# Kernel optimization log

Measured on AMD Instinct MI355X. Metric: run time of the kernel, lower is better.

Reference implementation:

```python
import jax, jax.numpy as jnp
import numpy as np

NUM_HEADS = 8
EPS = 1e-5


def conv3x3(x, w):
    # x: (b,c,f,w), w: (out_c,in_c,3,3), padding=1, stride=1, no bias
    return jax.lax.conv_general_dilated(
        x, w, window_strides=(1, 1), padding=((1, 1), (1, 1)),
        dimension_numbers=('NCHW', 'OIHW', 'NCHW'))


def mc_layernorm(x, g, b):
    # MultichannelLayerNorm: layernorm over the feature axis (dim 2),
    # per-(channel, feature) affine.
    m = jnp.mean(x, axis=2, keepdims=True)
    v = jnp.var(x, axis=2, keepdims=True)
    xn = (x - m) * jax.lax.rsqrt(v + EPS)
    return xn * g[None, :, :, None] + b[None, :, :, None]


def mc_linear(x, wp, wd=None):
    # per-channel feature linear: y[b,c,g,w] = sum_f wp[c,g,f] x[b,c,f,w]
    y = jnp.einsum('bcfw,cgf->bcgw', x, wp)
    if wd is not None:  # depthwise=True adds 1x1 cross-channel mix
        y = jnp.einsum('bcfw,oc->bofw', y, wd)
    return y


def _split_heads(t):
    # (b,c,f,w) -> (b,c,w,H,dh); matches transpose(2,3).reshape(b,c,w,H,-1)
    b, c, f, w = t.shape
    return jnp.transpose(t, (0, 1, 3, 2)).reshape(b, c, w, NUM_HEADS, f // NUM_HEADS)


def _forward(x, conv_q, conv_k, conv_v, wq, wk, wv, wo_pw, wo_dw,
             g1, b1, g2, b2, w1_pw, w1_dw, w2_pw):
    b, c, f, w = x.shape
    # --- attention (MultichannelMultiheadAttention, prev_qk=None) ---
    n1 = mc_layernorm(x, g1, b1)
    q = _split_heads(mc_linear(conv3x3(n1, conv_q), wq))  # (b,c,w,H,dh)
    k = _split_heads(mc_linear(conv3x3(n1, conv_k), wk))
    v = _split_heads(mc_linear(conv3x3(n1, conv_v), wv))
    # qk: (b,c,H,w,w); scaled by sqrt(features) (torch uses sqrt(h)=height)
    qk = jnp.einsum('bcqhd,bckhd->bchqk', q, k) / jnp.sqrt(jnp.float32(f))
    a = jnp.einsum('bchqk,bckhd->bcqhd', jax.nn.softmax(qk, axis=-1), v)
    a = jnp.transpose(a.reshape(b, c, w, f), (0, 1, 3, 2))  # (b,c,f,w)
    z = mc_linear(a, wo_pw, wo_dw)  # o_proj, depthwise=True
    h = x + z  # dropout is identity in eval
    # --- FFN with SquaredReLU ---
    n2 = mc_layernorm(h, g2, b2)
    u = mc_linear(n2, w1_pw, w1_dw)          # (b,c,4f,w)
    u = jnp.square(jax.nn.relu(u))           # SquaredReLU
    z = mc_linear(u, w2_pw)                  # (b,c,f,w)
    h = h + z
    return h, qk


def setup_inputs() -> dict:
    key = jax.random.key(0)
    ks = jax.random.split(key, 12)
    b, c, f, w = 2, 16, 256, 512
    e = 4 * f
    s_conv = 1.0 / np.sqrt(c * 9)
    s_f = 1.0 / np.sqrt(f)
    s_e = 1.0 / np.sqrt(e)
    s_c = 1.0 / np.sqrt(c)
    return {
        'x': jax.random.normal(ks[0], (b, c, f, w), jnp.float32),
        'conv_q': jax.random.normal(ks[1], (c, c, 3, 3), jnp.float32) * s_conv,
        'conv_k': jax.random.normal(ks[2], (c, c, 3, 3), jnp.float32) * s_conv,
        'conv_v': jax.random.normal(ks[3], (c, c, 3, 3), jnp.float32) * s_conv,
        'wq': jax.random.normal(ks[4], (c, f, f), jnp.float32) * s_f,
        'wk': jax.random.normal(ks[5], (c, f, f), jnp.float32) * s_f,
        'wv': jax.random.normal(ks[6], (c, f, f), jnp.float32) * s_f,
        'wo_pw': jax.random.normal(ks[7], (c, f, f), jnp.float32) * s_f,
        'wo_dw': jax.random.normal(ks[8], (c, c), jnp.float32) * s_c,
        'g1': jnp.ones((c, f), jnp.float32),
        'b1': jnp.zeros((c, f), jnp.float32),
        'g2': jnp.ones((c, f), jnp.float32),
        'b2': jnp.zeros((c, f), jnp.float32),
        'w1_pw': jax.random.normal(ks[9], (c, e, f), jnp.float32) * s_f,
        'w1_dw': jax.random.normal(ks[10], (c, c), jnp.float32) * s_c,
        'w2_pw': jax.random.normal(ks[11], (c, f, e), jnp.float32) * s_e,
    }


def reference(x, conv_q, conv_k, conv_v, wq, wk, wv, wo_pw, wo_dw,
              g1, b1, g2, b2, w1_pw, w1_dw, w2_pw):
    return _forward(x, conv_q, conv_k, conv_v, wq, wk, wv, wo_pw, wo_dw,
                    g1, b1, g2, b2, w1_pw, w1_dw, w2_pw)
```

## Files before the change

### kernel.cpp

```cpp
#include <hip/hip_runtime.h>

#define BB 2
#define CC 16
#define BC 32
#define FF 256
#define WW 512
#define HH 8
#define DH 32

using bf16x8 = __attribute__((ext_vector_type(8))) __bf16;
using f32x4  = __attribute__((ext_vector_type(4))) float;
using us8    = __attribute__((ext_vector_type(8))) unsigned short;
using us4    = __attribute__((ext_vector_type(4))) unsigned short;

#define AS1 __attribute__((address_space(1)))
#define AS3 __attribute__((address_space(3)))

__device__ __forceinline__ float bf2f(unsigned short u) {
    union { unsigned int i; float f; } x; x.i = ((unsigned int)u) << 16; return x.f;
}
__device__ __forceinline__ unsigned short f2bf(float f) {
    union { float f; unsigned int i; } x; x.f = f;
    unsigned int r = x.i + 0x7fffu + ((x.i >> 16) & 1u);
    return (unsigned short)(r >> 16);
}
__device__ __forceinline__ f32x4 mfma16(bf16x8 a, bf16x8 b, f32x4 c) {
    return __builtin_amdgcn_mfma_f32_16x16x32_bf16(a, b, c, 0, 0, 0);
}
__device__ __forceinline__ void gload16(const void* g, void* l) {
    __builtin_amdgcn_global_load_lds((AS1 void*)g, (AS3 void*)l, 16, 0, 0);
}

__global__ __launch_bounds__(256) void prep_ln(
    const float* __restrict__ x, const float* __restrict__ g1,
    const float* __restrict__ b1, unsigned short* __restrict__ n1,
    const float* __restrict__ wq, const float* __restrict__ wk,
    const float* __restrict__ wv, const float* __restrict__ wo,
    const float* __restrict__ w1, const float* __restrict__ w2,
    const float* __restrict__ cwq, const float* __restrict__ cwk,
    const float* __restrict__ cwv,
    unsigned short* __restrict__ Wqkv, unsigned short* __restrict__ Wo16,
    unsigned short* __restrict__ W116, unsigned short* __restrict__ W216,
    unsigned short* __restrict__ Aw) {
    __shared__ float red[2][8][32];
    __shared__ float mr[2][32];
    int bid = blockIdx.x;
    if (bid < 512) {
        int bc = bid & 31, c = bc & 15;
        int part = threadIdx.x >> 5, wl = threadIdx.x & 31;
        int w = (bid >> 5) * 32 + wl;
        const float* xp = x + ((size_t)bc * FF + part * 32) * WW + w;
        float s = 0.f, s2 = 0.f;
#pragma unroll 4
        for (int i = 0; i < 32; ++i) { float t = xp[(size_t)i * WW]; s += t; s2 += t * t; }
        red[0][part][wl] = s; red[1][part][wl] = s2;
        __syncthreads();
        if (part == 0) {
            float S = 0.f, S2 = 0.f;
#pragma unroll
            for (int p = 0; p < 8; ++p) { S += red[0][p][wl]; S2 += red[1][p][wl]; }
            float m = S * (1.f / FF);
            float v = S2 * (1.f / FF) - m * m;
            mr[0][wl] = m; mr[1][wl] = rsqrtf(v + 1e-5f);
        }
        __syncthreads();
        float m = mr[0][wl], r = mr[1][wl];
        const float* gp = g1 + c * FF + part * 32;
        const float* bp = b1 + c * FF + part * 32;
        unsigned short* op = n1 + ((size_t)bc * FF + part * 32) * WW + w;
#pragma unroll 4
        for (int i = 0; i < 32; ++i)
            op[(size_t)i * WW] = f2bf((xp[(size_t)i * WW] - m) * r * gp[i] + bp[i]);
    } else if (bid < 512 + 6144) {
        int i = (bid - 512) * 256 + threadIdx.x;
        const float* s; unsigned short* d; int off;
        if (i < 131072)       { s = wq; d = Wqkv;            off = i; }
        else if (i < 262144)  { s = wk; d = Wqkv + 1048576;  off = i - 131072; }
        else if (i < 393216)  { s = wv; d = Wqkv + 2097152;  off = i - 262144; }
        else if (i < 524288)  { s = wo; d = Wo16;            off = i - 393216; }
        else if (i < 1048576) { s = w1; d = W116;            off = i - 524288; }
        else                  { s = w2; d = W216;            off = i - 1048576; }
        const float4* sp = (const float4*)s + (size_t)off * 2;
        float4 a = sp[0], b = sp[1];
        us8 p;
        p[0] = f2bf(a.x); p[1] = f2bf(a.y); p[2] = f2bf(a.z); p[3] = f2bf(a.w);
        p[4] = f2bf(b.x); p[5] = f2bf(b.y); p[6] = f2bf(b.z); p[7] = f2bf(b.w);
        *((us8*)d + off) = p;
    } else {
        int idx = (bid - 512 - 6144) * 256 + threadIdx.x;
        if (idx < 7680) {
            int tensor = idx / 2560;
            int r = idx - tensor * 2560;
            int tp = r >> 9, co = (r >> 5) & 15, k = r & 31;
            int tap = tp * 2 + (k >> 4), ci = k & 15;
            float v = 0.f;
            if (tap < 9) {
                const float* w = tensor == 0 ? cwq : (tensor == 1 ? cwk : cwv);
                v = w[(co * 16 + ci) * 9 + tap];
            }
            Aw[idx] = f2bf(v);
        }
    }
}

__global__ __launch_bounds__(256) void ln2t_kernel(
    const float* __restrict__ x, const float* __restrict__ g,
    const float* __restrict__ bta, unsigned short* __restrict__ out) {
    __shared__ float red[2][8][32];
    __shared__ float mr[2][32];
    int bc = blockIdx.x, c = bc & 15;
    int part = threadIdx.x >> 5, wl = threadIdx.x & 31;
    int w = blockIdx.y * 32 + wl;
    const float* xp = x + ((size_t)bc * FF + part * 32) * WW + w;
    float s = 0.f, s2 = 0.f;
#pragma unroll 4
    for (int i = 0; i < 32; ++i) { float t = xp[(size_t)i * WW]; s += t; s2 += t * t; }
    red[0][part][wl] = s; red[1][part][wl] = s2;
    __syncthreads();
    if (part == 0) {
        float S = 0.f, S2 = 0.f;
#pragma unroll
        for (int p = 0; p < 8; ++p) { S += red[0][p][wl]; S2 += red[1][p][wl]; }
        float m = S * (1.f / FF);
        float v = S2 * (1.f / FF) - m * m;
        mr[0][wl] = m; mr[1][wl] = rsqrtf(v + 1e-5f);
    }
    __syncthreads();
    float m = mr[0][wl], r = mr[1][wl];
    const float* gp = g + c * FF + part * 32;
    const float* bp = bta + c * FF + part * 32;
    unsigned short* op = out + ((size_t)bc * WW + w) * FF + part * 32;
    for (int i8 = 0; i8 < 4; ++i8) {
        us8 pk;
#pragma unroll
        for (int e = 0; e < 8; ++e) {
            int i = i8 * 8 + e;
            pk[e] = f2bf((xp[(size_t)i * WW] - m) * r * gp[i] + bp[i]);
        }
        *(us8*)(op + i8 * 8) = pk;
    }
}

__global__ __launch_bounds__(256) void conv3_mfma(
    const unsigned short* __restrict__ n1, const unsigned short* __restrict__ Aw,
    unsigned short* __restrict__ oq, unsigned short* __restrict__ ok,
    unsigned short* __restrict__ ov) {
    __shared__ __align__(16) unsigned short Xl[6][68][16];
    const int b = blockIdx.z;
    const int f0 = blockIdx.y * 4;
    const int w0 = blockIdx.x * 64;
    const int tx = threadIdx.x;
    const int lane = tx & 63, wid = tx >> 6;
    const int lr = lane & 15, lg = lane >> 4;
    {
        uint4 z{0, 0, 0, 0};
        for (int i = tx; i < 816; i += 256) ((uint4*)Xl)[i] = z;
    }
    __syncthreads();
    if (tx < 240) {
        int c = tx % 10;
        int fr = (tx / 10) % 6;
        int ci0 = (tx / 60) * 4;
        int fy = f0 - 1 + fr;
        int wx = w0 - 8 + c * 8;
        if (fy >= 0 && fy < FF && wx >= 0 && wx <= WW - 8) {
            const unsigned short* base = n1 + ((size_t)(b * CC + ci0) * FF + fy) * WW + wx;
            us8 v0 = *(const us8*)(base);
            us8 v1 = *(const us8*)(base + (size_t)FF * WW);
            us8 v2 = *(const us8*)(base + (size_t)2 * FF * WW);
            us8 v3 = *(const us8*)(base + (size_t)3 * FF * WW);
            if (c >= 1 && c <= 8) {
#pragma unroll
                for (int e = 0; e < 8; ++e) {
                    int wl = c * 8 + e - 7;
                    us4 p; p.x = v0[e]; p.y = v1[e]; p.z = v2[e]; p.w = v3[e];
                    *(us4*)(&Xl[fr][wl][ci0]) = p;
                }
            } else {
#pragma unroll
                for (int e = 0; e < 8; ++e) {
                    int wl = c * 8 + e - 7;
                    if (wl >= 0 && wl < 66) {
                        us4 p; p.x = v0[e]; p.y = v1[e]; p.z = v2[e]; p.w = v3[e];
                        *(us4*)(&Xl[fr][wl][ci0]) = p;
                    }
                }
            }
        }
    }
    __syncthreads();
    bf16x8 A[3][5];
#pragma unroll
    for (int t3 = 0; t3 < 3; ++t3)
#pragma unroll
        for (int t = 0; t < 5; ++t)
            A[t3][t] = *(const bf16x8*)(Aw + ((t3 * 5 + t) * 16 + lr) * 32 + lg * 8);
    const bool h = (lane & 32) != 0;
    int doff[5];
    doff[0] = (h ? (-68 * 32) : ((-68 - 1) * 32));
    doff[1] = (h ? (-1 * 32) : ((-68 + 1) * 32));
    doff[2] = (h ? (1 * 32) : 0);
    doff[3] = (h ? (68 * 32) : ((68 - 1) * 32));
    doff[4] = ((68 + 1) * 32);
    const int fl = wid + 1;
    const int fglob = f0 + wid;
    char* xbase = (char*)Xl + (fl * 68 + 1) * 32 + ((lg & 1) ? 16 : 0);
#pragma unroll
    for (int pt = 0; pt < 4; ++pt) {
        char* bb = xbase + (pt * 16 + lr) * 32;
        bf16x8 Bf[5];
#pragma unroll
        for (int t = 0; t < 5; ++t) Bf[t] = *(const bf16x8*)(bb + doff[t]);
        f32x4 aq = {0.f, 0.f, 0.f, 0.f}, ak = {0.f, 0.f, 0.f, 0.f}, av = {0.f, 0.f, 0.f, 0.f};
#pragma unroll
        for (int t = 0; t < 5; ++t) {
            aq = mfma16(A[0][t], Bf[t], aq);
            ak = mfma16(A[1][t], Bf[t], ak);
            av = mfma16(A[2][t], Bf[t], av);
        }
        int w = w0 + pt * 16 + lr;
#pragma unroll
        for (int r = 0; r < 4; ++r) {
            int co = lg * 4 + r;
            size_t o = ((size_t)(b * CC + co) * FF + fglob) * WW + w;
            oq[o] = f2bf(aq[r]);
            ok[o] = f2bf(ak[r]);
            ov[o] = f2bf(av[r]);
        }
    }
}

template <int K, int BSRC, int MODE, int NT>
__global__ __launch_bounds__(256, 3) void mgemm3(
    const unsigned short* __restrict__ Wb, const unsigned short* __restrict__ T,
    unsigned short* __restrict__ ob, float* __restrict__ of) {
    constexpr int M = 256;
    constexpr int NK = K / 64;
    __shared__ __align__(16) unsigned short Al[2][64 * 64];
    __shared__ __align__(16) unsigned short Bl[2][128 * 64];
    const int id = blockIdx.x;
    const int grp = ((id >> 5) << 3) | (id & 7);
    const int g = (id >> 3) & 3;
    const int t = (NT > 1) ? (grp >> 7) : 0;
    const int rem = grp & 127;
    const int bc = rem >> 2, z = rem & 3;
    const int c = bc & 15;
    const int G0 = g * 64, W0 = z * 128;
    const int tx = threadIdx.x;
    const int lane = tx & 63, wid = tx >> 6;
    const int lr = lane & 15, lg = lane >> 4;
    const int wr = wid >> 1, wc = wid & 1;
    const unsigned short* Ab = Wb + (size_t)t * 1048576 + ((size_t)c * M + G0) * K;
    const unsigned short* Tt = T + (size_t)t * 4194304;
    const unsigned short* TbB0 = Tt + ((size_t)bc * WW + W0) * K;
    const unsigned short* TbB1 = Tt + (size_t)bc * K * WW;
    const int arow0 = tx >> 3;
    const int wseg = tx & 15, fgrp = tx >> 4;
    f32x4 acc[2][4];
#pragma unroll
    for (int i = 0; i < 2; ++i)
#pragma unroll
        for (int j = 0; j < 4; ++j) acc[i][j] = (f32x4){0.f, 0.f, 0.f, 0.f};

#define STAGE_A(buf, f0)                                                     \
    _Pragma("unroll")                                                        \
    for (int rep = 0; rep < 2; ++rep) {                                      \
        int row = arow0 + rep * 32;                                          \
        int seg = (tx & 7) ^ (row & 7);                                      \
        gload16(Ab + (size_t)row * K + (f0) + seg * 8,                       \
                (char*)Al[buf] + wid * 1024 + rep * 4096);                   \
    }
#define STAGE_B0(buf, f0)                                                    \
    _Pragma("unroll")                                                        \
    for (int rep = 0; rep < 4; ++rep) {                                      \
        int row = arow0 + rep * 32;                                          \
        int seg = (tx & 7) ^ (row & 7) ^ ((row >> 3) & 7);                   \
        gload16(TbB0 + (size_t)row * K + (f0) + seg * 8,                     \
                (char*)Bl[buf] + wid * 1024 + rep * 4096);                   \
    }
#define GATHER_B1(f0)                                                        \
    _Pragma("unroll")                                                        \
    for (int i = 0; i < 4; ++i)                                              \
        tv[i] = *(const us8*)(TbB1 + (size_t)((f0) + fgrp * 4 + i) * WW + W0 + wseg * 8);
#define WRITE_B1(buf)                                                        \
    _Pragma("unroll")                                                        \
    for (int j = 0; j < 8; ++j) {                                            \
        int w = wseg * 8 + j;                                                \
        us4 p; p.x = tv[0][j]; p.y = tv[1][j]; p.z = tv[2][j]; p.w = tv[3][j]; \
        *(us4*)((char*)Bl[buf] + w * 128 +                                   \
                ((((fgrp >> 1) ^ (w & 7) ^ ((w >> 3) & 7)) << 4)) + (fgrp & 1) * 8) = p; \
    }

    us8 tv[4];
    STAGE_A(0, 0)
    if (BSRC == 0) { STAGE_B0(0, 0) } else { GATHER_B1(0) WRITE_B1(0) }
    __syncthreads();
    int cur = 0;
    for (int k = 0; k < NK; ++k) {
        const int f0n = (k + 1) * 64;
        if (k + 1 < NK) {
            STAGE_A(cur ^ 1, f0n)
            if (BSRC == 0) { STAGE_B0(cur ^ 1, f0n) }
            else { GATHER_B1(f0n) }
        }
#pragma unroll
        for (int kc = 0; kc < 2; ++kc) {
            bf16x8 af[2], bf[4];
#pragma unroll
            for (int i = 0; i < 2; ++i) {
                int gr = wr * 32 + i * 16 + lr;
                af[i] = *(const bf16x8*)((char*)Al[cur] + gr * 128 +
                        (((kc * 4 + lg) ^ (gr & 7)) << 4));
            }
#pragma unroll
            for (int j = 0; j < 4; ++j) {
                int wrw = wc * 64 + j * 16 + lr;
                bf[j] = *(const bf16x8*)((char*)Bl[cur] + wrw * 128 +
                        (((kc * 4 + lg) ^ (wrw & 7) ^ ((wrw >> 3) & 7)) << 4));
            }
#pragma unroll
            for (int i = 0; i < 2; ++i)
#pragma unroll
                for (int j = 0; j < 4; ++j)
                    acc[i][j] = mfma16(af[i], bf[j], acc[i][j]);
        }
        if (BSRC == 1 && k + 1 < NK) { WRITE_B1(cur ^ 1) }
        __syncthreads();
        cur ^= 1;
    }
#undef STAGE_A
#undef STAGE_B0
#undef GATHER_B1
#undef WRITE_B1
#pragma unroll
    for (int i = 0; i < 2; ++i)
#pragma unroll
        for (int j = 0; j < 4; ++j) {
            int g2 = G0 + wr * 32 + i * 16 + lg * 4;
            int w = W0 + wc * 64 + j * 16 + lr;
#pragma unroll
            for (int r = 0; r < 4; ++r) {
                size_t o = (size_t)t * 4194304 + ((size_t)bc * M + g2 + r) * WW + w;
                if (MODE == 0) ob[o] = f2bf(acc[i][j][r]);
                else of[o] += acc[i][j][r];
            }
        }
}

template <int K, int M, int MODE>
__global__ __launch_bounds__(256, 2) void mgemm2(
    const unsigned short* __restrict__ Wb, const unsigned short* __restrict__ T,
    unsigned short* __restrict__ ob, float* __restrict__ of) {
    __shared__ __align__(16) unsigned short SH[2][128 * 64];
    unsigned short* Al = SH[0];
    unsigned short* Bl = SH[1];
    const int id = blockIdx.x;
    const int grp = ((id >> 6) << 3) | (id & 7);
    const int g = (id >> 3) & 7;
    const int bc = grp >> 2, z = grp & 3;
    const int c = bc & 15;
    const int G0 = g * 128, W0 = z * 128;
    const int tx = threadIdx.x;
    const int lane = tx & 63, wid = tx >> 6;
    const int lr = lane & 15, lg = lane >> 4;
    const int wr = wid >> 1, wc = wid & 1;
    const unsigned short* Ab = Wb + ((size_t)c * M + G0) * K;
    f32x4 acc[4][4];
#pragma unroll
    for (int i = 0; i < 4; ++i)
#pragma unroll
        for (int j = 0; j < 4; ++j) acc[i][j] = (f32x4){0.f, 0.f, 0.f, 0.f};

    const int arow0 = tx >> 3;

    for (int f0 = 0; f0 < K; f0 += 64) {
#pragma unroll
        for (int rep = 0; rep < 4; ++rep) {
            int row = arow0 + rep * 32;
            int seg = (tx & 7) ^ (row & 7);
            gload16(Ab + (size_t)row * K + f0 + seg * 8,
                    (char*)Al + wid * 1024 + rep * 4096);
        }
        {
            const unsigned short* Tb = T + ((size_t)bc * WW + W0) * K;
#pragma unroll
            for (int rep = 0; rep < 4; ++rep) {
                int row = arow0 + rep * 32;
                int seg = (tx & 7) ^ (row & 7) ^ ((row >> 3) & 7);
                gload16(Tb + (size_t)row * K + f0 + seg * 8,
                        (char*)Bl + wid * 1024 + rep * 4096);
            }
        }
        __syncthreads();
#pragma unroll
        for (int kc = 0; kc < 2; ++kc) {
            bf16x8 af[4], bf[4];
#pragma unroll
            for (int i = 0; i < 4; ++i) {
                int gr = wr * 64 + i * 16 + lr;
                af[i] = *(const bf16x8*)((char*)Al + gr * 128 +
                        (((kc * 4 + lg) ^ (gr & 7)) << 4));
                int wrw = wc * 64 + i * 16 + lr;
                bf[i] = *(const bf16x8*)((char*)Bl + wrw * 128 +
                        (((kc * 4 + lg) ^ (wrw & 7) ^ ((wrw >> 3) & 7)) << 4));
            }
#pragma unroll
            for (int i = 0; i < 4; ++i)
#pragma unroll
                for (int j = 0; j < 4; ++j)
                    acc[i][j] = mfma16(af[i], bf[j], acc[i][j]);
        }
        __syncthreads();
    }
    if (MODE == 2) {
        char* S = (char*)SH;
#pragma unroll
        for (int i = 0; i < 4; ++i)
#pragma unroll
            for (int j = 0; j < 4; ++j) {
                int wl = wc * 64 + j * 16 + lr;
                int gl = wr * 64 + i * 16 + lg * 4;
                us4 pk;
                pk.x = f2bf(acc[i][j][0]); pk.y = f2bf(acc[i][j][1]);
                pk.z = f2bf(acc[i][j][2]); pk.w = f2bf(acc[i][j][3]);
                *(us4*)(S + wl * 256 + ((gl * 2) ^ ((wl & 7) << 4))) = pk;
            }
        __syncthreads();
        unsigned short* og = ob + ((size_t)bc * WW + W0) * M + G0;
#pragma unroll
        for (int rep = 0; rep < 8; ++rep) {
            int slot = tx + rep * 256;
            int row = slot >> 4, col = slot & 15;
            us8 v = *(const us8*)(S + row * 256 + ((col * 16) ^ ((row & 7) << 4)));
            *(us8*)(og + (size_t)row * M + col * 8) = v;
        }
    } else {
#pragma unroll
        for (int i = 0; i < 4; ++i)
#pragma unroll
            for (int j = 0; j < 4; ++j) {
                int gg = G0 + wr * 64 + i * 16 + lg * 4;
                int w = W0 + wc * 64 + j * 16 + lr;
#pragma unroll
                for (int r = 0; r < 4; ++r) {
                    size_t o = ((size_t)bc * M + gg + r) * WW + w;
                    if (MODE == 0) ob[o] = f2bf(acc[i][j][r]);
                    else of[o] += acc[i][j][r];
                }
            }
    }
}

__global__ __launch_bounds__(256, 2) void attn_fused(
    const unsigned short* __restrict__ qb, const unsigned short* __restrict__ kb,
    const unsigned short* __restrict__ vb, float* __restrict__ qko,
    unsigned short* __restrict__ abT) {
    __shared__ unsigned short Kl[512 * 32];
    __shared__ unsigned short Ql[64 * 32];
    const int bch = blockIdx.x, qt = blockIdx.y;
    const int bc = bch >> 3, h = bch & 7;
    const int tx = threadIdx.x;
    const int lane = tx & 63, wid = tx >> 6;
    const int lr = lane & 15, lg = lane >> 4;

    const unsigned short* kbase = kb + ((size_t)bc * FF + h * DH) * WW;
    const unsigned short* vbase = vb + ((size_t)bc * FF + h * DH) * WW;
    const unsigned short* qbase = qb + ((size_t)bc * FF + h * DH) * WW + qt * 64;

    {
        int d0 = ((tx >> 3) & 7) * 4;
#pragma unroll
        for (int rep = 0; rep < 2; ++rep) {
            int kw0 = (tx & 7) * 8 + ((tx >> 6) & 3) * 64 + rep * 256;
            us8 v0 = *(const us8*)(kbase + (size_t)(d0 + 0) * WW + kw0);
            us8 v1 = *(const us8*)(kbase + (size_t)(d0 + 1) * WW + kw0);
            us8 v2 = *(const us8*)(kbase + (size_t)(d0 + 2) * WW + kw0);
            us8 v3 = *(const us8*)(kbase + (size_t)(d0 + 3) * WW + kw0);
#pragma unroll
            for (int j = 0; j < 8; ++j) {
                int kw = kw0 + j;
                us4 p; p.x = v0[j]; p.y = v1[j]; p.z = v2[j]; p.w = v3[j];
                *(us4*)((char*)Kl + kw * 64 + ((d0 * 2) ^ ((kw & 3) << 4))) = p;
            }
        }
    }
    if (tx < 64) {
        int d0 = ((tx >> 3) & 7) * 4;
        int q0 = (tx & 7) * 8;
        us8 v0 = *(const us8*)(qbase + (size_t)(d0 + 0) * WW + q0);
        us8 v1 = *(const us8*)(qbase + (size_t)(d0 + 1) * WW + q0);
        us8 v2 = *(const us8*)(qbase + (size_t)(d0 + 2) * WW + q0);
        us8 v3 = *(const us8*)(qbase + (size_t)(d0 + 3) * WW + q0);
#pragma unroll
        for (int j = 0; j < 8; ++j) {
            us4 p; p.x = v0[j]; p.y = v1[j]; p.z = v2[j]; p.w = v3[j];
            *(us4*)(&Ql[(q0 + j) * 32 + d0]) = p;
        }
    }
    __syncthreads();

    const int q0w = wid * 16;
    bf16x8 qf = *(const bf16x8*)((char*)Ql + (q0w + lr) * 64 + lg * 16);
    f32x4 s[32];
#pragma unroll
    for (int i = 0; i < 32; ++i) s[i] = (f32x4){0.f, 0.f, 0.f, 0.f};
#pragma unroll
    for (int kwt = 0; kwt < 32; ++kwt) {
        int krow = kwt * 16 + lr;
        bf16x8 kf = *(const bf16x8*)((char*)Kl + krow * 64 + ((lg * 16) ^ ((krow & 3) << 4)));
        s[kwt] = mfma16(kf, qf, s[kwt]);
    }
    float mx = -3.0e38f;
    float* qrow = qko + ((size_t)bch * WW + qt * 64 + q0w + lr) * WW;
#pragma unroll
    for (int kwt = 0; kwt < 32; ++kwt) {
        s[kwt] *= 0.0625f;
        float4 st;
        st.x = s[kwt][0]; st.y = s[kwt][1]; st.z = s[kwt][2]; st.w = s[kwt][3];
        *(float4*)(qrow + kwt * 16 + lg * 4) = st;
        mx = fmaxf(mx, fmaxf(fmaxf(st.x, st.y), fmaxf(st.z, st.w)));
    }
    mx = fmaxf(mx, __shfl_xor(mx, 16));
    mx = fmaxf(mx, __shfl_xor(mx, 32));
    float sum = 0.f;
#pragma unroll
    for (int kwt = 0; kwt < 32; ++kwt) {
#pragma unroll
        for (int r = 0; r < 4; ++r) {
            float p = __expf(s[kwt][r] - mx);
            s[kwt][r] = p;
            sum += p;
        }
    }
    sum += __shfl_xor(sum, 16);
    sum += __shfl_xor(sum, 32);
    float inv = 1.0f / sum;

    f32x4 av[2];
    av[0] = (f32x4){0.f, 0.f, 0.f, 0.f};
    av[1] = (f32x4){0.f, 0.f, 0.f, 0.f};
#pragma unroll
    for (int t = 0; t < 16; ++t) {
        unsigned pa0 = f2bf(s[2 * t][0]) | ((unsigned)f2bf(s[2 * t][1]) << 16);
        unsigned pa1 = f2bf(s[2 * t][2]) | ((unsigned)f2bf(s[2 * t][3]) << 16);
        unsigned pb0 = f2bf(s[2 * t + 1][0]) | ((unsigned)f2bf(s[2 * t + 1][1]) << 16);
        unsigned pb1 = f2bf(s[2 * t + 1][2]) | ((unsigned)f2bf(s[2 * t + 1][3]) << 16);
        unsigned s16_0 = (lg == 1) ? pa0 : pb0, s16_1 = (lg == 1) ? pa1 : pb1;
        unsigned s32_0 = (lg == 3) ? pa0 : pb0, s32_1 = (lg == 3) ? pa1 : pb1;
        unsigned s48_0 = (lg == 2) ? pa0 : pb0, s48_1 = (lg == 2) ? pa1 : pb1;
        unsigned r16_0 = (unsigned)__shfl_xor((int)s16_0, 16);
        unsigned r16_1 = (unsigned)__shfl_xor((int)s16_1, 16);
        unsigned r32_0 = (unsigned)__shfl_xor((int)s32_0, 32);
        unsigned r32_1 = (unsigned)__shfl_xor((int)s32_1, 32);
        unsigned r48_0 = (unsigned)__shfl_xor((int)s48_0, 48);
        unsigned r48_1 = (unsigned)__shfl_xor((int)s48_1, 48);
        uint4 wv;
        if (lg == 0)      { wv.x = pa0;   wv.y = pa1;   wv.z = r16_0; wv.w = r16_1; }
        else if (lg == 1) { wv.x = r48_0; wv.y = r48_1; wv.z = r32_0; wv.w = r32_1; }
        else if (lg == 2) { wv.x = r32_0; wv.y = r32_1; wv.z = r48_0; wv.w = r48_1; }
        else              { wv.x = r16_0; wv.y = r16_1; wv.z = pb0;  wv.w = pb1; }
        bf16x8 pf = *reinterpret_cast<bf16x8*>(&wv);
#pragma unroll
        for (int di = 0; di < 2; ++di) {
            int vr = di * 16 + lr;
            bf16x8 vf = *(const bf16x8*)(vbase + (size_t)vr * WW + t * 32 + lg * 8);
            av[di] = mfma16(vf, pf, av[di]);
        }
    }
    unsigned short* arow = abT + ((size_t)bc * WW + qt * 64 + q0w + lr) * FF + h * DH;
#pragma unroll
    for (int di = 0; di < 2; ++di) {
        us4 pk;
        pk.x = f2bf(av[di][0] * inv); pk.y = f2bf(av[di][1] * inv);
        pk.z = f2bf(av[di][2] * inv); pk.w = f2bf(av[di][3] * inv);
        *(us4*)(arow + di * 16 + lg * 4) = pk;
    }
}

template <int NPC, int MODE, int TILE>
__global__ __launch_bounds__(256) void dwmix(
    const unsigned short* __restrict__ in, const float* __restrict__ wdw,
    const float* __restrict__ x, float* __restrict__ fo, unsigned short* __restrict__ bo) {
    __shared__ unsigned short L[16][TILE];
    constexpr int C8 = TILE / 8;
    constexpr int LV = TILE / 128;
    constexpr int PER = TILE / 256;
    int b = blockIdx.y;
    size_t base = (size_t)blockIdx.x * TILE;
    int tx = threadIdx.x;
#pragma unroll
    for (int r = 0; r < LV; ++r) {
        int idx = tx + r * 256;
        int ci = idx / C8;
        int seg = idx % C8;
        *(us8*)&L[ci][seg * 8] = *(const us8*)(in + ((size_t)(b * 16 + ci)) * NPC + base + seg * 8);
    }
    __syncthreads();
#pragma unroll
    for (int pos = 0; pos < PER; ++pos) {
        int fw = tx + pos * 256;
        float vin[16];
#pragma unroll
        for (int ci = 0; ci < 16; ++ci) vin[ci] = bf2f(L[ci][fw]);
#pragma unroll
        for (int o = 0; o < 16; ++o) {
            float s = 0.f;
#pragma unroll
            for (int ci = 0; ci < 16; ++ci) s += wdw[o * 16 + ci] * vin[ci];
            size_t oi = ((size_t)(b * 16 + o)) * NPC + base + fw;
            if (MODE == 0) fo[oi] = x[oi] + s;
            else { s = fmaxf(s, 0.f); bo[oi] = f2bf(s * s); }
        }
    }
}

extern "C" void kernel_launch(void* const* d_in, const int* in_sizes, int n_in,
                              void* d_out, int out_size, void* d_ws, size_t ws_size,
                              hipStream_t stream) {
    const float* x      = (const float*)d_in[0];
    const float* conv_q = (const float*)d_in[1];
    const float* conv_k = (const float*)d_in[2];
    const float* conv_v = (const float*)d_in[3];
    const float* wq     = (const float*)d_in[4];
    const float* wk     = (const float*)d_in[5];
    const float* wv     = (const float*)d_in[6];
    const float* wo_pw  = (const float*)d_in[7];
    const float* wo_dw  = (const float*)d_in[8];
    const float* g1     = (const float*)d_in[9];
    const float* b1     = (const float*)d_in[10];
    const float* g2     = (const float*)d_in[11];
    const float* b2     = (const float*)d_in[12];
    const float* w1_pw  = (const float*)d_in[13];
    const float* w1_dw  = (const float*)d_in[14];
    const float* w2_pw  = (const float*)d_in[15];

    float* hout  = (float*)d_out;
    float* qkout = (float*)d_out + 4194304;

    char* ws = (char*)d_ws;
    const size_t MB1 = (size_t)1 << 20;
    unsigned short* n1   = (unsigned short*)(ws + 0 * MB1);
    unsigned short* cq   = (unsigned short*)(ws + 8 * MB1);
    unsigned short* qb   = (unsigned short*)(ws + 32 * MB1);
    unsigned short* kb   = (unsigned short*)(ws + 40 * MB1);
    unsigned short* vb   = (unsigned short*)(ws + 48 * MB1);
    unsigned short* abT  = (unsigned short*)(ws + 56 * MB1);
    unsigned short* pwb  = (unsigned short*)(ws + 64 * MB1);
    unsigned short* n2t  = (unsigned short*)(ws + 72 * MB1);
    unsigned short* u1t  = (unsigned short*)(ws + 80 * MB1);
    unsigned short* u2t  = (unsigned short*)(ws + 112 * MB1);
    unsigned short* Wqkv = (unsigned short*)(ws + 144 * MB1);
    unsigned short* Wo16 = (unsigned short*)(ws + 150 * MB1);
    unsigned short* W116 = (unsigned short*)(ws + 152 * MB1);
    unsigned short* W216 = (unsigned short*)(ws + 160 * MB1);
    unsigned short* Awb  = (unsigned short*)(ws + 168 * MB1);

    prep_ln<<<dim3(6686), 256, 0, stream>>>(x, g1, b1, n1,
                                            wq, wk, wv, wo_pw, w1_pw, w2_pw,
                                            conv_q, conv_k, conv_v,
                                            Wqkv, Wo16, W116, W216, Awb);
    conv3_mfma<<<dim3(8, 64, BB), 256, 0, stream>>>(n1, Awb, cq, cq + 4194304, cq + 8388608);
    mgemm3<256, 1, 0, 3><<<dim3(1536), 256, 0, stream>>>(Wqkv, cq, qb, nullptr);
    attn_fused<<<dim3(BC * HH, 8), 256, 0, stream>>>(qb, kb, vb, qkout, abT);
    mgemm3<256, 0, 0, 1><<<dim3(512), 256, 0, stream>>>(Wo16, abT, pwb, nullptr);
    dwmix<131072, 0, 256><<<dim3(512, BB), 256, 0, stream>>>(pwb, wo_dw, x, hout, nullptr);
    ln2t_kernel<<<dim3(BC, 16), 256, 0, stream>>>(hout, g2, b2, n2t);
    mgemm2<256, 1024, 2><<<dim3(1024), 256, 0, stream>>>(W116, n2t, u1t, nullptr);
    dwmix<524288, 1, 1024><<<dim3(512, BB), 256, 0, stream>>>(u1t, w1_dw, nullptr, nullptr, u2t);
    mgemm3<1024, 0, 1, 1><<<dim3(512), 256, 0, stream>>>(W216, u2t, nullptr, hout);
}
```

Before: 261.8 us.

## Unify per-channel GEMMs into templated mgemm4 with configurable W tile width

Replaces mgemm3 and mgemm2 with one templated kernel parameterised by W tile width (128 or 256) and number of 64-row output groups. The QKV projection now uses 256-wide W tiles, with a wider transposing gather that packs 8 feature rows per LDS store, halving the grid. The FFN up-projection moves from a 128x128 single-buffered tile to a double-buffered 64x256 tile with a transposed bf16 epilogue through LDS. The larger B tiles raise LDS use and registers per block, and occupancy drops to 2 blocks per CU for the 256-wide variants.

New measurement: 267.2 us. +2.0%, slower.

```diff
diff --git a/kernel.cpp b/kernel.cpp
--- a/kernel.cpp
+++ b/kernel.cpp
@@ -230,82 +230,112 @@
     }
 }
 
-template <int K, int BSRC, int MODE, int NT>
-__global__ __launch_bounds__(256, 3) void mgemm3(
+template <int K, int WT, int BSRC, int MODE, int NT, int NG>
+__global__ __launch_bounds__(256, (WT == 256 ? 2 : 3)) void mgemm4(
     const unsigned short* __restrict__ Wb, const unsigned short* __restrict__ T,
     unsigned short* __restrict__ ob, float* __restrict__ of) {
-    constexpr int M = 256;
+    constexpr int M = NG * 64;
     constexpr int NK = K / 64;
+    constexpr int GB = (NG == 16 ? 4 : 2);
+    constexpr int ZB = (WT == 256 ? 1 : 2);
+    constexpr int JN = WT / 32;
+    constexpr int BREPS = WT / 32;
     __shared__ __align__(16) unsigned short Al[2][64 * 64];
-    __shared__ __align__(16) unsigned short Bl[2][128 * 64];
+    __shared__ __align__(16) unsigned short Bl[2][WT * 64];
     const int id = blockIdx.x;
-    const int grp = ((id >> 5) << 3) | (id & 7);
-    const int g = (id >> 3) & 3;
-    const int t = (NT > 1) ? (grp >> 7) : 0;
-    const int rem = grp & 127;
-    const int bc = rem >> 2, z = rem & 3;
+    const int grp = ((id >> (3 + GB)) << 3) | (id & 7);
+    const int g = (id >> 3) & (NG - 1);
+    const int t = (NT > 1) ? (grp >> (5 + ZB)) : 0;
+    const int rem = grp & ((32 << ZB) - 1);
+    const int bc = rem >> ZB, z = rem & ((1 << ZB) - 1);
     const int c = bc & 15;
-    const int G0 = g * 64, W0 = z * 128;
+    const int G0 = g * 64, W0 = z * WT;
     const int tx = threadIdx.x;
     const int lane = tx & 63, wid = tx >> 6;
     const int lr = lane & 15, lg = lane >> 4;
     const int wr = wid >> 1, wc = wid & 1;
-    const unsigned short* Ab = Wb + (size_t)t * 1048576 + ((size_t)c * M + G0) * K;
+    const unsigned short* Ab = Wb + (size_t)t * (M * 16 * K) + ((size_t)c * M + G0) * K;
     const unsigned short* Tt = T + (size_t)t * 4194304;
     const unsigned short* TbB0 = Tt + ((size_t)bc * WW + W0) * K;
     const unsigned short* TbB1 = Tt + (size_t)bc * K * WW;
     const int arow0 = tx >> 3;
-    const int wseg = tx & 15, fgrp = tx >> 4;
-    f32x4 acc[2][4];
+    f32x4 acc[2][JN];
 #pragma unroll
     for (int i = 0; i < 2; ++i)
 #pragma unroll
-        for (int j = 0; j < 4; ++j) acc[i][j] = (f32x4){0.f, 0.f, 0.f, 0.f};
-
-#define STAGE_A(buf, f0)                                                     \
-    _Pragma("unroll")                                                        \
-    for (int rep = 0; rep < 2; ++rep) {                                      \
-        int row = arow0 + rep * 32;                                          \
-        int seg = (tx & 7) ^ (row & 7);                                      \
-        gload16(Ab + (size_t)row * K + (f0) + seg * 8,                       \
-                (char*)Al[buf] + wid * 1024 + rep * 4096);                   \
-    }
-#define STAGE_B0(buf, f0)                                                    \
-    _Pragma("unroll")                                                        \
-    for (int rep = 0; rep < 4; ++rep) {                                      \
-        int row = arow0 + rep * 32;                                          \
-        int seg = (tx & 7) ^ (row & 7) ^ ((row >> 3) & 7);                   \
-        gload16(TbB0 + (size_t)row * K + (f0) + seg * 8,                     \
-                (char*)Bl[buf] + wid * 1024 + rep * 4096);                   \
-    }
-#define GATHER_B1(f0)                                                        \
-    _Pragma("unroll")                                                        \
-    for (int i = 0; i < 4; ++i)                                              \
-        tv[i] = *(const us8*)(TbB1 + (size_t)((f0) + fgrp * 4 + i) * WW + W0 + wseg * 8);
-#define WRITE_B1(buf)                                                        \
-    _Pragma("unroll")                                                        \
-    for (int j = 0; j < 8; ++j) {                                            \
-        int w = wseg * 8 + j;                                                \
-        us4 p; p.x = tv[0][j]; p.y = tv[1][j]; p.z = tv[2][j]; p.w = tv[3][j]; \
-        *(us4*)((char*)Bl[buf] + w * 128 +                                   \
-                ((((fgrp >> 1) ^ (w & 7) ^ ((w >> 3) & 7)) << 4)) + (fgrp & 1) * 8) = p; \
-    }
-
-    us8 tv[4];
-    STAGE_A(0, 0)
-    if (BSRC == 0) { STAGE_B0(0, 0) } else { GATHER_B1(0) WRITE_B1(0) }
+        for (int j = 0; j < JN; ++j) acc[i][j] = (f32x4){0.f, 0.f, 0.f, 0.f};
+
+    us8 tv[8];
+
+    auto stageA = [&](int buf, int f0) {
+#pragma unroll
+        for (int rep = 0; rep < 2; ++rep) {
+            int row = arow0 + rep * 32;
+            int seg = (tx & 7) ^ (row & 7);
+            gload16(Ab + (size_t)row * K + f0 + seg * 8,
+                    (char*)Al[buf] + wid * 1024 + rep * 4096);
+        }
+    };
+    auto stageB0 = [&](int buf, int f0) {
+#pragma unroll
+        for (int rep = 0; rep < BREPS; ++rep) {
+            int row = arow0 + rep * 32;
+            int seg = (tx & 7) ^ (row & 7) ^ ((row >> 3) & 7);
+            gload16(TbB0 + (size_t)row * K + f0 + seg * 8,
+                    (char*)Bl[buf] + wid * 1024 + rep * 4096);
+        }
+    };
+    auto gatherB1 = [&](int f0) {
+        if (WT == 128) {
+            const int wseg = tx & 15, fgrp = tx >> 4;
+#pragma unroll
+            for (int i = 0; i < 4; ++i)
+                tv[i] = *(const us8*)(TbB1 + (size_t)(f0 + fgrp * 4 + i) * WW + W0 + wseg * 8);
+        } else {
+            const int wseg = tx & 31, fgrp = tx >> 5;
+#pragma unroll
+            for (int i = 0; i < 8; ++i)
+                tv[i] = *(const us8*)(TbB1 + (size_t)(f0 + fgrp * 8 + i) * WW + W0 + wseg * 8);
+        }
+    };
+    auto writeB1 = [&](int buf) {
+        if (WT == 128) {
+            const int wseg = tx & 15, fgrp = tx >> 4;
+#pragma unroll
+            for (int j = 0; j < 8; ++j) {
+                int w = wseg * 8 + j;
+                us4 p; p.x = tv[0][j]; p.y = tv[1][j]; p.z = tv[2][j]; p.w = tv[3][j];
+                *(us4*)((char*)Bl[buf] + w * 128 +
+                        ((((fgrp >> 1) ^ (w & 7) ^ ((w >> 3) & 7)) << 4)) + (fgrp & 1) * 8) = p;
+            }
+        } else {
+            const int wseg = tx & 31, fgrp = tx >> 5;
+#pragma unroll
+            for (int j = 0; j < 8; ++j) {
+                int w = wseg * 8 + j;
+                us8 p;
+#pragma unroll
+                for (int i = 0; i < 8; ++i) p[i] = tv[i][j];
+                *(us8*)((char*)Bl[buf] + w * 128 +
+                        (((fgrp ^ (w & 7) ^ ((w >> 3) & 7)) << 4))) = p;
+            }
+        }
+    };
+
+    stageA(0, 0);
+    if (BSRC == 0) { stageB0(0, 0); } else { gatherB1(0); writeB1(0); }
     __syncthreads();
     int cur = 0;
     for (int k = 0; k < NK; ++k) {
         const int f0n = (k + 1) * 64;
         if (k + 1 < NK) {
-            STAGE_A(cur ^ 1, f0n)
-            if (BSRC == 0) { STAGE_B0(cur ^ 1, f0n) }
-            else { GATHER_B1(f0n) }
+            stageA(cur ^ 1, f0n);
+            if (BSRC == 0) { stageB0(cur ^ 1, f0n); }
+            else { gatherB1(f0n); }
         }
 #pragma unroll
         for (int kc = 0; kc < 2; ++kc) {
-            bf16x8 af[2], bf[4];
+            bf16x8 af[2], bf[JN];
 #pragma unroll
             for (int i = 0; i < 2; ++i) {
                 int gr = wr * 32 + i * 16 + lr;
@@ -313,137 +343,54 @@
                         (((kc * 4 + lg) ^ (gr & 7)) << 4));
             }
 #pragma unroll
-            for (int j = 0; j < 4; ++j) {
-                int wrw = wc * 64 + j * 16 + lr;
+            for (int j = 0; j < JN; ++j) {
+                int wrw = wc * (WT / 2) + j * 16 + lr;
                 bf[j] = *(const bf16x8*)((char*)Bl[cur] + wrw * 128 +
                         (((kc * 4 + lg) ^ (wrw & 7) ^ ((wrw >> 3) & 7)) << 4));
             }
 #pragma unroll
             for (int i = 0; i < 2; ++i)
 #pragma unroll
-                for (int j = 0; j < 4; ++j)
+                for (int j = 0; j < JN; ++j)
                     acc[i][j] = mfma16(af[i], bf[j], acc[i][j]);
         }
-        if (BSRC == 1 && k + 1 < NK) { WRITE_B1(cur ^ 1) }
+        if (BSRC == 1 && k + 1 < NK) { writeB1(cur ^ 1); }
         __syncthreads();
         cur ^= 1;
     }
-#undef STAGE_A
-#undef STAGE_B0
-#undef GATHER_B1
-#undef WRITE_B1
-#pragma unroll
-    for (int i = 0; i < 2; ++i)
-#pragma unroll
-        for (int j = 0; j < 4; ++j) {
-            int g2 = G0 + wr * 32 + i * 16 + lg * 4;
-            int w = W0 + wc * 64 + j * 16 + lr;
-#pragma unroll
-            for (int r = 0; r < 4; ++r) {
-                size_t o = (size_t)t * 4194304 + ((size_t)bc * M + g2 + r) * WW + w;
-                if (MODE == 0) ob[o] = f2bf(acc[i][j][r]);
-                else of[o] += acc[i][j][r];
-            }
-        }
-}
-
-template <int K, int M, int MODE>
-__global__ __launch_bounds__(256, 2) void mgemm2(
-    const unsigned short* __restrict__ Wb, const unsigned short* __restrict__ T,
-    unsigned short* __restrict__ ob, float* __restrict__ of) {
-    __shared__ __align__(16) unsigned short SH[2][128 * 64];
-    unsigned short* Al = SH[0];
-    unsigned short* Bl = SH[1];
-    const int id = blockIdx.x;
-    const int grp = ((id >> 6) << 3) | (id & 7);
-    const int g = (id >> 3) & 7;
-    const int bc = grp >> 2, z = grp & 3;
-    const int c = bc & 15;
-    const int G0 = g * 128, W0 = z * 128;
-    const int tx = threadIdx.x;
-    const int lane = tx & 63, wid = tx >> 6;
-    const int lr = lane & 15, lg = lane >> 4;
-    const int wr = wid >> 1, wc = wid & 1;
-    const unsigned short* Ab = Wb + ((size_t)c * M + G0) * K;
-    f32x4 acc[4][4];
-#pragma unroll
-    for (int i = 0; i < 4; ++i)
-#pragma unroll
-        for (int j = 0; j < 4; ++j) acc[i][j] = (f32x4){0.f, 0.f, 0.f, 0.f};
-
-    const int arow0 = tx >> 3;
-
-    for (int f0 = 0; f0 < K; f0 += 64) {
-#pragma unroll
-        for (int rep = 0; rep < 4; ++rep) {
-            int row = arow0 + rep * 32;
-            int seg = (tx & 7) ^ (row & 7);
-            gload16(Ab + (size_t)row * K + f0 + seg * 8,
-                    (char*)Al + wid * 1024 + rep * 4096);
-        }
-        {
-            const unsigned short* Tb = T + ((size_t)bc * WW + W0) * K;
-#pragma unroll
-            for (int rep = 0; rep < 4; ++rep) {
-                int row = arow0 + rep * 32;
-                int seg = (tx & 7) ^ (row & 7) ^ ((row >> 3) & 7);
-                gload16(Tb + (size_t)row * K + f0 + seg * 8,
-                        (char*)Bl + wid * 1024 + rep * 4096);
-            }
-        }
-        __syncthreads();
-#pragma unroll
-        for (int kc = 0; kc < 2; ++kc) {
-            bf16x8 af[4], bf[4];
-#pragma unroll
-            for (int i = 0; i < 4; ++i) {
-                int gr = wr * 64 + i * 16 + lr;
-                af[i] = *(const bf16x8*)((char*)Al + gr * 128 +
-                        (((kc * 4 + lg) ^ (gr & 7)) << 4));
-                int wrw = wc * 64 + i * 16 + lr;
-                bf[i] = *(const bf16x8*)((char*)Bl + wrw * 128 +
-                        (((kc * 4 + lg) ^ (wrw & 7) ^ ((wrw >> 3) & 7)) << 4));
-            }
-#pragma unroll
-            for (int i = 0; i < 4; ++i)
-#pragma unroll
-                for (int j = 0; j < 4; ++j)
-                    acc[i][j] = mfma16(af[i], bf[j], acc[i][j]);
-        }
-        __syncthreads();
-    }
+
     if (MODE == 2) {
-        char* S = (char*)SH;
-#pragma unroll
-        for (int i = 0; i < 4; ++i)
-#pragma unroll
-            for (int j = 0; j < 4; ++j) {
-                int wl = wc * 64 + j * 16 + lr;
-                int gl = wr * 64 + i * 16 + lg * 4;
+        char* S = (char*)Bl;
+#pragma unroll
+        for (int i = 0; i < 2; ++i)
+#pragma unroll
+            for (int j = 0; j < JN; ++j) {
+                int wl = wc * (WT / 2) + j * 16 + lr;
+                int gl = wr * 32 + i * 16 + lg * 4;
                 us4 pk;
                 pk.x = f2bf(acc[i][j][0]); pk.y = f2bf(acc[i][j][1]);
                 pk.z = f2bf(acc[i][j][2]); pk.w = f2bf(acc[i][j][3]);
-                *(us4*)(S + wl * 256 + ((gl * 2) ^ ((wl & 7) << 4))) = pk;
+                *(us4*)(S + wl * 128 + ((gl * 2) ^ ((wl & 7) << 4))) = pk;
             }
         __syncthreads();
-        unsigned short* og = ob + ((size_t)bc * WW + W0) * M + G0;
-#pragma unroll
-        for (int rep = 0; rep < 8; ++rep) {
+        constexpr int OREPS = WT * 128 / 4096;
+#pragma unroll
+        for (int rep = 0; rep < OREPS; ++rep) {
             int slot = tx + rep * 256;
-            int row = slot >> 4, col = slot & 15;
-            us8 v = *(const us8*)(S + row * 256 + ((col * 16) ^ ((row & 7) << 4)));
-            *(us8*)(og + (size_t)row * M + col * 8) = v;
+            int row = slot >> 3, seg = slot & 7;
+            us8 v = *(const us8*)(S + row * 128 + (((seg ^ (row & 7)) << 4)));
+            *(us8*)(ob + ((size_t)bc * WW + W0 + row) * M + G0 + seg * 8) = v;
         }
     } else {
 #pragma unroll
-        for (int i = 0; i < 4; ++i)
-#pragma unroll
-            for (int j = 0; j < 4; ++j) {
-                int gg = G0 + wr * 64 + i * 16 + lg * 4;
-                int w = W0 + wc * 64 + j * 16 + lr;
+        for (int i = 0; i < 2; ++i)
+#pragma unroll
+            for (int j = 0; j < JN; ++j) {
+                int g2 = G0 + wr * 32 + i * 16 + lg * 4;
+                int w = W0 + wc * (WT / 2) + j * 16 + lr;
 #pragma unroll
                 for (int r = 0; r < 4; ++r) {
-                    size_t o = ((size_t)bc * M + gg + r) * WW + w;
+                    size_t o = (size_t)t * 4194304 + ((size_t)bc * M + g2 + r) * WW + w;
                     if (MODE == 0) ob[o] = f2bf(acc[i][j][r]);
                     else of[o] += acc[i][j][r];
                 }
@@ -660,12 +607,12 @@
                                             conv_q, conv_k, conv_v,
                                             Wqkv, Wo16, W116, W216, Awb);
     conv3_mfma<<<dim3(8, 64, BB), 256, 0, stream>>>(n1, Awb, cq, cq + 4194304, cq + 8388608);
-    mgemm3<256, 1, 0, 3><<<dim3(1536), 256, 0, stream>>>(Wqkv, cq, qb, nullptr);
+    mgemm4<256, 256, 1, 0, 3, 4><<<dim3(768), 256, 0, stream>>>(Wqkv, cq, qb, nullptr);
     attn_fused<<<dim3(BC * HH, 8), 256, 0, stream>>>(qb, kb, vb, qkout, abT);
-    mgemm3<256, 0, 0, 1><<<dim3(512), 256, 0, stream>>>(Wo16, abT, pwb, nullptr);
+    mgemm4<256, 128, 0, 0, 1, 4><<<dim3(512), 256, 0, stream>>>(Wo16, abT, pwb, nullptr);
     dwmix<131072, 0, 256><<<dim3(512, BB), 256, 0, stream>>>(pwb, wo_dw, x, hout, nullptr);
     ln2t_kernel<<<dim3(BC, 16), 256, 0, stream>>>(hout, g2, b2, n2t);
-    mgemm2<256, 1024, 2><<<dim3(1024), 256, 0, stream>>>(W116, n2t, u1t, nullptr);
+    mgemm4<256, 256, 0, 2, 1, 16><<<dim3(1024), 256, 0, stream>>>(W116, n2t, u1t, nullptr);
     dwmix<524288, 1, 1024><<<dim3(512, BB), 256, 0, stream>>>(u1t, w1_dw, nullptr, nullptr, u2t);
-    mgemm3<1024, 0, 1, 1><<<dim3(512), 256, 0, stream>>>(W216, u2t, nullptr, hout);
-}
+    mgemm4<1024, 128, 0, 1, 1, 4><<<dim3(512), 256, 0, stream>>>(W216, u2t, nullptr, hout);
+}
```
